# Optimization experiments

Hardware: AMD Instinct MI355X
Metric: run time of the kernel (lower is better)

The kernel has to match this reference:

```python
import jax, jax.numpy as jnp
import numpy as np
from jax import lax

C = 384        # in_channels
K = 16         # number of frames selected (self.k)
SIGMA = 0.05   # perturbation sigma (forward arg, hardcoded)
NUM_SAMPLES = 500


def setup_inputs() -> dict:
    key = jax.random.key(0)
    ks = jax.random.split(key, 8)
    B, T, N = 16, 32, 196
    D = 2 * C  # PredictorLG embed_dim for 'tpool'
    w = lambda k, s: jax.random.normal(k, s, jnp.float32) * 0.02
    return {
        "x": jax.random.normal(ks[0], (B, T * N, C), jnp.float32),
        "noise": jax.random.normal(ks[1], (B, NUM_SAMPLES, T), jnp.float32),
        "ln_g": jnp.ones((D,), jnp.float32),
        "ln_b": jnp.zeros((D,), jnp.float32),
        "w_in": w(ks[2], (D, D)), "b_in": jnp.zeros((D,), jnp.float32),
        "w1": w(ks[3], (D, D // 2)), "b1": jnp.zeros((D // 2,), jnp.float32),
        "w2": w(ks[4], (D // 2, D // 4)), "b2": jnp.zeros((D // 4,), jnp.float32),
        "w3": w(ks[5], (D // 4, 1)), "b3": jnp.zeros((1,), jnp.float32),
        "N": N, "T": T,
    }


def _predictor(x_, ln_g, ln_b, w_in, b_in, w1, b1, w2, b2, w3, b3):
    # PredictorLG: LayerNorm -> Linear -> GELU -> local/global split -> MLP -> scalar score
    mu = x_.mean(-1, keepdims=True)
    var = x_.var(-1, keepdims=True)  # biased, matches nn.LayerNorm
    h = (x_ - mu) / jnp.sqrt(var + 1e-5) * ln_g + ln_b
    h = jax.nn.gelu(h @ w_in + b_in, approximate=False)
    half = h.shape[-1] // 2
    g = h[..., half:].mean(axis=1, keepdims=True)                      # global pool over T
    h = jnp.concatenate([h[..., :half], jnp.broadcast_to(g, h[..., :half].shape)], -1)
    h = jax.nn.gelu(h @ w1 + b1, approximate=False)
    h = jax.nn.gelu(h @ w2 + b2, approximate=False)
    return (h @ w3 + b3)[..., 0]                                       # (B, T)


def reference(x, noise, ln_g, ln_b, w_in, b_in, w1, b1, w2, b2, w3, b3, N, T):
    B = x.shape[0]
    xt = x.reshape(B, T, N, C)                                         # b t n c
    x_ = jnp.concatenate([xt.mean(2), xt.max(2)], -1)                  # (B, T, 2C)
    scores = _predictor(x_, ln_g, ln_b, w_in, b_in, w1, b1, w2, b2, w3, b3)
    lo = scores.min(-1, keepdims=True)
    hi = scores.max(-1, keepdims=True)
    scores = (scores - lo) / (hi - lo + 1e-5)                          # min_max_norm
    # PerturbedTopKFunction.forward
    perturbed = scores[:, None, :] + noise * SIGMA                     # (B, ns, T)
    idx = jnp.sort(lax.top_k(perturbed, K)[1], axis=-1)                # (B, ns, K)
    indicators = jax.nn.one_hot(idx, T, dtype=x.dtype).mean(1)         # (B, K, T)
    # extract_patches_from_indicators: einsum over flattened frames
    patches = jnp.einsum('bkt,btc->bkc', indicators, xt.reshape(B, T, N * C))
    return patches.reshape(B, K * N, C)                                # 'b k (n c) -> b (k n) c'
```

## Files before the change

kernel.cpp:

```cpp
#include <hip/hip_runtime.h>
#include <math.h>

#define CC 384
#define DD 768
#define TT 32
#define NN 196
#define BB 16
#define KK 16
#define NSAMP 500
#define JV 18816
#define FRAME 75264

__device__ __forceinline__ float gelu_exact(float x) {
    return 0.5f * x * (1.0f + erff(x * 0.70710678118654752440f));
}

__global__ __launch_bounds__(384) void pool_kernel(const float* __restrict__ x,
                                                   const float* __restrict__ ln_g,
                                                   const float* __restrict__ ln_b,
                                                   float* __restrict__ xbar) {
    int row = blockIdx.x;
    const float4* xp = (const float4*)(x + (size_t)row * NN * CC);
    int tx = threadIdx.x;
    int ty = threadIdx.y;
    float4 s = make_float4(0.f, 0.f, 0.f, 0.f);
    float4 m = make_float4(-INFINITY, -INFINITY, -INFINITY, -INFINITY);
    for (int n = ty; n < NN; n += 4) {
        float4 v = xp[n * 96 + tx];
        s.x += v.x; s.y += v.y; s.z += v.z; s.w += v.w;
        m.x = fmaxf(m.x, v.x); m.y = fmaxf(m.y, v.y);
        m.z = fmaxf(m.z, v.z); m.w = fmaxf(m.w, v.w);
    }
    __shared__ float4 ssum[4][96];
    __shared__ float4 smax[4][96];
    __shared__ float xf[DD];
    ssum[ty][tx] = s;
    smax[ty][tx] = m;
    __syncthreads();
    if (ty == 0) {
        for (int r = 1; r < 4; ++r) {
            float4 a = ssum[r][tx];
            s.x += a.x; s.y += a.y; s.z += a.z; s.w += a.w;
            float4 b = smax[r][tx];
            m.x = fmaxf(m.x, b.x); m.y = fmaxf(m.y, b.y);
            m.z = fmaxf(m.z, b.z); m.w = fmaxf(m.w, b.w);
        }
        const float invn = 1.0f / (float)NN;
        xf[4*tx+0] = s.x * invn; xf[4*tx+1] = s.y * invn;
        xf[4*tx+2] = s.z * invn; xf[4*tx+3] = s.w * invn;
        xf[CC + 4*tx+0] = m.x; xf[CC + 4*tx+1] = m.y;
        xf[CC + 4*tx+2] = m.z; xf[CC + 4*tx+3] = m.w;
    }
    __syncthreads();
    int tid = ty * 96 + tx;
    float e0 = xf[tid], e1 = xf[tid + CC];
    float ps = e0 + e1, pq = e0 * e0 + e1 * e1;
    #pragma unroll
    for (int off = 32; off; off >>= 1) {
        ps += __shfl_down(ps, off);
        pq += __shfl_down(pq, off);
    }
    __shared__ float red[12];
    __shared__ float mv[2];
    int wv = tid >> 6;
    if ((tid & 63) == 0) { red[wv] = ps; red[6 + wv] = pq; }
    __syncthreads();
    if (tid == 0) {
        float su = 0.f, sq = 0.f;
        #pragma unroll
        for (int i = 0; i < 6; ++i) { su += red[i]; sq += red[6 + i]; }
        float mean = su * (1.0f / DD);
        float var  = sq * (1.0f / DD) - mean * mean;
        mv[0] = mean;
        mv[1] = rsqrtf(var + 1e-5f);
    }
    __syncthreads();
    float mean = mv[0], inv = mv[1];
    float* o = xbar + (size_t)row * DD;
    o[tid]      = (e0 - mean) * inv * ln_g[tid]      + ln_b[tid];
    o[tid + CC] = (e1 - mean) * inv * ln_g[tid + CC] + ln_b[tid + CC];
}

__global__ __launch_bounds__(1024) void fcin_kernel(const float* __restrict__ xbar,
                                                    const float* __restrict__ w_in,
                                                    const float* __restrict__ b_in,
                                                    float* __restrict__ h1,
                                                    float* __restrict__ Gpart) {
    __shared__ float xs[4][DD];
    __shared__ float pacc[4][4][256];
    int tid = threadIdx.x;
    int rowg = blockIdx.x;
    int row0 = rowg * 4;
    int col0 = blockIdx.y * 256;

    if (tid < 768) {
        int r = tid / 192, j = tid % 192;
        ((float4*)xs[r])[j] = *(const float4*)(xbar + (size_t)(row0 + r) * DD + 4 * j);
    }
    __syncthreads();

    int kg = tid >> 8;
    int c  = tid & 255;
    int col = col0 + c;
    int k0 = kg * 192;
    float a0 = 0.f, a1 = 0.f, a2 = 0.f, a3 = 0.f;
    const float* wp = w_in + (size_t)k0 * DD + col;
    #pragma unroll 2
    for (int i = 0; i < 192; i += 4) {
        float w0 = wp[(size_t)(i + 0) * DD];
        float w1v = wp[(size_t)(i + 1) * DD];
        float w2v = wp[(size_t)(i + 2) * DD];
        float w3v = wp[(size_t)(i + 3) * DD];
        float4 x0 = *(const float4*)&xs[0][k0 + i];
        float4 x1 = *(const float4*)&xs[1][k0 + i];
        float4 x2 = *(const float4*)&xs[2][k0 + i];
        float4 x3 = *(const float4*)&xs[3][k0 + i];
        a0 += x0.x * w0 + x0.y * w1v + x0.z * w2v + x0.w * w3v;
        a1 += x1.x * w0 + x1.y * w1v + x1.z * w2v + x1.w * w3v;
        a2 += x2.x * w0 + x2.y * w1v + x2.z * w2v + x2.w * w3v;
        a3 += x3.x * w0 + x3.y * w1v + x3.z * w2v + x3.w * w3v;
    }
    pacc[kg][0][c] = a0; pacc[kg][1][c] = a1;
    pacc[kg][2][c] = a2; pacc[kg][3][c] = a3;
    __syncthreads();

    int rr = tid >> 8;
    float s = b_in[col] + pacc[0][rr][c] + pacc[1][rr][c]
                        + pacc[2][rr][c] + pacc[3][rr][c];
    float g = gelu_exact(s);
    h1[(size_t)(row0 + rr) * DD + col] = g;
    pacc[0][rr][c] = g;
    __syncthreads();

    if (rr == 0 && col >= CC) {
        float gsum = pacc[0][0][c] + pacc[0][1][c] + pacc[0][2][c] + pacc[0][3][c];
        Gpart[(size_t)rowg * CC + (col - CC)] = gsum;
    }
}

__global__ __launch_bounds__(768) void mlp1_kernel(const float* __restrict__ h1,
                                                   const float* __restrict__ Gpart,
                                                   const float* __restrict__ w1,
                                                   const float* __restrict__ b1,
                                                   float* __restrict__ h2) {
    __shared__ float xs[4][CC];
    __shared__ float gs[CC];
    __shared__ float pacc[4][5][192];
    int tid = threadIdx.x;
    int rowg = blockIdx.x;
    int row0 = rowg * 4;
    int b = row0 >> 5;
    int col0 = blockIdx.y * 192;

    if (tid < CC) {
        float s = 0.f;
        const float* gp = Gpart + (size_t)(b * 8) * CC + tid;
        #pragma unroll
        for (int rg = 0; rg < 8; ++rg) s += gp[(size_t)rg * CC];
        gs[tid] = s * (1.0f / 32.0f);
    } else {
        int e = tid - CC;
        int r = e / 96, j = e % 96;
        ((float4*)xs[r])[j] = *(const float4*)(h1 + (size_t)(row0 + r) * DD + 4 * j);
    }
    __syncthreads();

    int kg = tid / 192;
    int c  = tid % 192;
    int col = col0 + c;
    int k0 = kg * 96;
    float a0 = 0.f, a1 = 0.f, a2 = 0.f, a3 = 0.f, ag = 0.f;
    const float* wl = w1 + (size_t)k0 * CC + col;
    const float* wg = w1 + (size_t)(CC + k0) * CC + col;
    #pragma unroll 2
    for (int i = 0; i < 96; i += 4) {
        float l0 = wl[(size_t)(i + 0) * CC];
        float l1 = wl[(size_t)(i + 1) * CC];
        float l2 = wl[(size_t)(i + 2) * CC];
        float l3 = wl[(size_t)(i + 3) * CC];
        float g0 = wg[(size_t)(i + 0) * CC];
        float g1 = wg[(size_t)(i + 1) * CC];
        float g2 = wg[(size_t)(i + 2) * CC];
        float g3 = wg[(size_t)(i + 3) * CC];
        float4 x0 = *(const float4*)&xs[0][k0 + i];
        float4 x1 = *(const float4*)&xs[1][k0 + i];
        float4 x2 = *(const float4*)&xs[2][k0 + i];
        float4 x3 = *(const float4*)&xs[3][k0 + i];
        float4 gv = *(const float4*)&gs[k0 + i];
        a0 += x0.x * l0 + x0.y * l1 + x0.z * l2 + x0.w * l3;
        a1 += x1.x * l0 + x1.y * l1 + x1.z * l2 + x1.w * l3;
        a2 += x2.x * l0 + x2.y * l1 + x2.z * l2 + x2.w * l3;
        a3 += x3.x * l0 + x3.y * l1 + x3.z * l2 + x3.w * l3;
        ag += gv.x * g0 + gv.y * g1 + gv.z * g2 + gv.w * g3;
    }
    pacc[kg][0][c] = a0; pacc[kg][1][c] = a1;
    pacc[kg][2][c] = a2; pacc[kg][3][c] = a3;
    pacc[kg][4][c] = ag;
    __syncthreads();

    int rr = tid / 192;
    float s = b1[col];
    #pragma unroll
    for (int kk = 0; kk < 4; ++kk)
        s += pacc[kk][rr][c] + pacc[kk][4][c];
    h2[(size_t)(row0 + rr) * CC + col] = gelu_exact(s);
}

__global__ __launch_bounds__(192) void score_kernel(const float* __restrict__ h2,
                                                    const float* __restrict__ w2,
                                                    const float* __restrict__ b2,
                                                    const float* __restrict__ w3,
                                                    float* __restrict__ scores) {
    __shared__ float h2row[CC];
    int row = blockIdx.x, tid = threadIdx.x;

    if (tid < 96)
        ((float4*)h2row)[tid] = ((const float4*)(h2 + (size_t)row * CC))[tid];
    __syncthreads();

    float a = b2[tid];
    const float* wp = w2 + tid;
    #pragma unroll 8
    for (int k = 0; k < CC; ++k)
        a += h2row[k] * wp[(size_t)k * 192];
    float v = gelu_exact(a) * w3[tid];
    #pragma unroll
    for (int off = 32; off; off >>= 1) v += __shfl_down(v, off);
    __shared__ float red[3];
    if ((tid & 63) == 0) red[tid >> 6] = v;
    __syncthreads();
    if (tid == 0) scores[row] = red[0] + red[1] + red[2];
}

__global__ __launch_bounds__(512) void topk_kernel(const float* __restrict__ scores,
                                                   const float* __restrict__ noise,
                                                   float* __restrict__ ind) {
    __shared__ float ns[TT];
    __shared__ float mnmx[2];
    __shared__ int counts[KK * TT];
    int b = blockIdx.x, tid = threadIdx.x;

    if (tid < TT) ns[tid] = scores[b * TT + tid];
    counts[tid] = 0;
    __syncthreads();
    if (tid == 0) {
        float mn = ns[0], mx = ns[0];
        for (int t = 1; t < TT; ++t) { mn = fminf(mn, ns[t]); mx = fmaxf(mx, ns[t]); }
        mnmx[0] = mn; mnmx[1] = mx;
    }
    __syncthreads();
    if (tid < TT) ns[tid] = (ns[tid] - mnmx[0]) / (mnmx[1] - mnmx[0] + 1e-5f);
    __syncthreads();

    if (tid < NSAMP) {
        const float* nb = noise + ((size_t)b * NSAMP + tid) * TT;
        float p[TT];
        #pragma unroll
        for (int t = 0; t < TT; ++t) p[t] = ns[t] + nb[t] * 0.05f;
        int k = 0;
        #pragma unroll
        for (int t = 0; t < TT; ++t) {
            int rank = 0;
            #pragma unroll
            for (int u = 0; u < TT; ++u)
                rank += (p[u] > p[t] || (p[u] == p[t] && u < t)) ? 1 : 0;
            if (rank < KK) { atomicAdd(&counts[k * TT + t], 1); ++k; }
        }
    }
    __syncthreads();
    ind[b * (KK * TT) + tid] = (float)counts[tid] * (1.0f / NSAMP);
}

__global__ __launch_bounds__(256) void gather_kernel(const float* __restrict__ x,
                                                     const float* __restrict__ ind,
                                                     float* __restrict__ out) {
    __shared__ float w[KK * TT];
    __shared__ int act[TT];
    __shared__ int nact_s;
    int b = blockIdx.y;
    int tid = threadIdx.x;
    w[tid] = ind[b * (KK * TT) + tid];
    w[256 + tid] = ind[b * (KK * TT) + 256 + tid];
    __syncthreads();
    if (tid < TT) {
        float s = 0.f;
        #pragma unroll
        for (int k = 0; k < KK; ++k) s += w[k * TT + tid];
        unsigned long long m = __ballot(s != 0.f);
        if (s != 0.f) act[__popcll(m & ((1ull << tid) - 1ull))] = tid;
        if (tid == 0) nact_s = (int)__popcll(m);
    }
    __syncthreads();
    int nact = nact_s;

    int j4 = blockIdx.x * 256 + tid;
    if (j4 >= JV) return;

    const float4* xb = (const float4*)(x + (size_t)b * TT * FRAME);
    float4 acc[KK];
    #pragma unroll
    for (int k = 0; k < KK; ++k) acc[k] = make_float4(0.f, 0.f, 0.f, 0.f);

    for (int it = 0; it < nact; ++it) {
        int t = act[it];
        float4 v = xb[(size_t)t * JV + j4];
        #pragma unroll
        for (int k = 0; k < KK; ++k) {
            float wk = w[k * TT + t];
            acc[k].x += wk * v.x; acc[k].y += wk * v.y;
            acc[k].z += wk * v.z; acc[k].w += wk * v.w;
        }
    }
    float4* ob = (float4*)(out + (size_t)b * KK * FRAME);
    #pragma unroll
    for (int k = 0; k < KK; ++k)
        ob[(size_t)k * JV + j4] = acc[k];
}

extern "C" void kernel_launch(void* const* d_in, const int* in_sizes, int n_in,
                              void* d_out, int out_size, void* d_ws, size_t ws_size,
                              hipStream_t stream) {
    const float* x     = (const float*)d_in[0];
    const float* noise = (const float*)d_in[1];
    const float* ln_g  = (const float*)d_in[2];
    const float* ln_b  = (const float*)d_in[3];
    const float* w_in  = (const float*)d_in[4];
    const float* b_in  = (const float*)d_in[5];
    const float* w1    = (const float*)d_in[6];
    const float* b1    = (const float*)d_in[7];
    const float* w2    = (const float*)d_in[8];
    const float* b2    = (const float*)d_in[9];
    const float* w3    = (const float*)d_in[10];
    const float* b3    = (const float*)d_in[11];
    (void)b3;
    float* out = (float*)d_out;

    float* ws     = (float*)d_ws;
    float* xbar   = ws;
    float* h1     = xbar + 512 * DD;
    float* Gpart  = h1 + 512 * DD;
    float* h2     = Gpart + 128 * CC;
    float* scores = h2 + 512 * CC;
    float* ind    = scores + 512;

    hipLaunchKernelGGL(pool_kernel, dim3(BB * TT), dim3(96, 4), 0, stream,
                       x, ln_g, ln_b, xbar);
    hipLaunchKernelGGL(fcin_kernel, dim3(128, 3), dim3(1024), 0, stream,
                       xbar, w_in, b_in, h1, Gpart);
    hipLaunchKernelGGL(mlp1_kernel, dim3(128, 2), dim3(768), 0, stream,
                       h1, Gpart, w1, b1, h2);
    hipLaunchKernelGGL(score_kernel, dim3(512), dim3(192), 0, stream,
                       h2, w2, b2, w3, scores);
    hipLaunchKernelGGL(topk_kernel, dim3(BB), dim3(512), 0, stream,
                       scores, noise, ind);
    hipLaunchKernelGGL(gather_kernel, dim3((JV + 255) / 256, BB), dim3(256), 0, stream,
                       x, ind, out);
}
```

Before: 120.4 us.

## Fuse MLP layers with scoring and fold top-k into gather kernel

Merges the mlp1 and score kernels into one kernel that processes two rows per block and keeps h2 in shared memory. It also moves the perturbed top-k indicator computation into every gather block, so the separate topk kernel and its ind buffer go away. The aim is to cut two kernel launches and the global round-trips for h2 and the indicators. In exchange, every gather block (74 per batch) redundantly recomputes top-k over 500 samples, and the w1 and w2 weights are re-read by each of 256 blocks.

Result: slower. 136.8 us (+13.6%).

```diff
diff --git a/kernel.cpp b/kernel.cpp
--- a/kernel.cpp
+++ b/kernel.cpp
@@ -138,19 +138,23 @@
     }
 }
 
-__global__ __launch_bounds__(768) void mlp1_kernel(const float* __restrict__ h1,
-                                                   const float* __restrict__ Gpart,
-                                                   const float* __restrict__ w1,
-                                                   const float* __restrict__ b1,
-                                                   float* __restrict__ h2) {
-    __shared__ float xs[4][CC];
+__global__ __launch_bounds__(768) void mlp1score_kernel(const float* __restrict__ h1,
+                                                        const float* __restrict__ Gpart,
+                                                        const float* __restrict__ w1,
+                                                        const float* __restrict__ b1,
+                                                        const float* __restrict__ w2,
+                                                        const float* __restrict__ b2,
+                                                        const float* __restrict__ w3,
+                                                        float* __restrict__ scores) {
     __shared__ float gs[CC];
-    __shared__ float pacc[4][5][192];
+    __shared__ float xs[2][CC];
+    __shared__ float pacc[2][3][CC];
+    __shared__ float h2s[2][CC];
+    __shared__ float sacc[2][2][192];
+    __shared__ float red[2][3];
     int tid = threadIdx.x;
-    int rowg = blockIdx.x;
-    int row0 = rowg * 4;
+    int row0 = blockIdx.x * 2;
     int b = row0 >> 5;
-    int col0 = blockIdx.y * 192;
 
     if (tid < CC) {
         float s = 0.f;
@@ -158,90 +162,95 @@
         #pragma unroll
         for (int rg = 0; rg < 8; ++rg) s += gp[(size_t)rg * CC];
         gs[tid] = s * (1.0f / 32.0f);
-    } else {
+    } else if (tid < CC + 192) {
         int e = tid - CC;
         int r = e / 96, j = e % 96;
         ((float4*)xs[r])[j] = *(const float4*)(h1 + (size_t)(row0 + r) * DD + 4 * j);
     }
     __syncthreads();
 
-    int kg = tid / 192;
-    int c  = tid % 192;
-    int col = col0 + c;
-    int k0 = kg * 96;
-    float a0 = 0.f, a1 = 0.f, a2 = 0.f, a3 = 0.f, ag = 0.f;
-    const float* wl = w1 + (size_t)k0 * CC + col;
-    const float* wg = w1 + (size_t)(CC + k0) * CC + col;
-    #pragma unroll 2
-    for (int i = 0; i < 96; i += 4) {
-        float l0 = wl[(size_t)(i + 0) * CC];
-        float l1 = wl[(size_t)(i + 1) * CC];
-        float l2 = wl[(size_t)(i + 2) * CC];
-        float l3 = wl[(size_t)(i + 3) * CC];
-        float g0 = wg[(size_t)(i + 0) * CC];
-        float g1 = wg[(size_t)(i + 1) * CC];
-        float g2 = wg[(size_t)(i + 2) * CC];
-        float g3 = wg[(size_t)(i + 3) * CC];
-        float4 x0 = *(const float4*)&xs[0][k0 + i];
-        float4 x1 = *(const float4*)&xs[1][k0 + i];
-        float4 x2 = *(const float4*)&xs[2][k0 + i];
-        float4 x3 = *(const float4*)&xs[3][k0 + i];
-        float4 gv = *(const float4*)&gs[k0 + i];
-        a0 += x0.x * l0 + x0.y * l1 + x0.z * l2 + x0.w * l3;
-        a1 += x1.x * l0 + x1.y * l1 + x1.z * l2 + x1.w * l3;
-        a2 += x2.x * l0 + x2.y * l1 + x2.z * l2 + x2.w * l3;
-        a3 += x3.x * l0 + x3.y * l1 + x3.z * l2 + x3.w * l3;
-        ag += gv.x * g0 + gv.y * g1 + gv.z * g2 + gv.w * g3;
-    }
-    pacc[kg][0][c] = a0; pacc[kg][1][c] = a1;
-    pacc[kg][2][c] = a2; pacc[kg][3][c] = a3;
-    pacc[kg][4][c] = ag;
-    __syncthreads();
-
-    int rr = tid / 192;
-    float s = b1[col];
-    #pragma unroll
-    for (int kk = 0; kk < 4; ++kk)
-        s += pacc[kk][rr][c] + pacc[kk][4][c];
-    h2[(size_t)(row0 + rr) * CC + col] = gelu_exact(s);
-}
-
-__global__ __launch_bounds__(192) void score_kernel(const float* __restrict__ h2,
-                                                    const float* __restrict__ w2,
-                                                    const float* __restrict__ b2,
-                                                    const float* __restrict__ w3,
-                                                    float* __restrict__ scores) {
-    __shared__ float h2row[CC];
-    int row = blockIdx.x, tid = threadIdx.x;
-
-    if (tid < 96)
-        ((float4*)h2row)[tid] = ((const float4*)(h2 + (size_t)row * CC))[tid];
-    __syncthreads();
-
-    float a = b2[tid];
-    const float* wp = w2 + tid;
-    #pragma unroll 8
-    for (int k = 0; k < CC; ++k)
-        a += h2row[k] * wp[(size_t)k * 192];
-    float v = gelu_exact(a) * w3[tid];
-    #pragma unroll
-    for (int off = 32; off; off >>= 1) v += __shfl_down(v, off);
-    __shared__ float red[3];
-    if ((tid & 63) == 0) red[tid >> 6] = v;
-    __syncthreads();
-    if (tid == 0) scores[row] = red[0] + red[1] + red[2];
-}
-
-__global__ __launch_bounds__(512) void topk_kernel(const float* __restrict__ scores,
-                                                   const float* __restrict__ noise,
-                                                   float* __restrict__ ind) {
+    {
+        int kg = tid / CC;
+        int col = tid % CC;
+        int k0 = kg * 192;
+        float a0 = 0.f, a1 = 0.f, ag = 0.f;
+        const float* wl = w1 + (size_t)k0 * CC + col;
+        const float* wg = w1 + (size_t)(CC + k0) * CC + col;
+        #pragma unroll 2
+        for (int i = 0; i < 192; i += 4) {
+            float l0 = wl[(size_t)(i + 0) * CC];
+            float l1 = wl[(size_t)(i + 1) * CC];
+            float l2 = wl[(size_t)(i + 2) * CC];
+            float l3 = wl[(size_t)(i + 3) * CC];
+            float g0 = wg[(size_t)(i + 0) * CC];
+            float g1 = wg[(size_t)(i + 1) * CC];
+            float g2 = wg[(size_t)(i + 2) * CC];
+            float g3 = wg[(size_t)(i + 3) * CC];
+            float4 x0 = *(const float4*)&xs[0][k0 + i];
+            float4 x1 = *(const float4*)&xs[1][k0 + i];
+            float4 gv = *(const float4*)&gs[k0 + i];
+            a0 += x0.x * l0 + x0.y * l1 + x0.z * l2 + x0.w * l3;
+            a1 += x1.x * l0 + x1.y * l1 + x1.z * l2 + x1.w * l3;
+            ag += gv.x * g0 + gv.y * g1 + gv.z * g2 + gv.w * g3;
+        }
+        pacc[kg][0][col] = a0;
+        pacc[kg][1][col] = a1;
+        pacc[kg][2][col] = ag;
+    }
+    __syncthreads();
+
+    {
+        int rr = tid / CC;
+        int c2 = tid % CC;
+        float s = b1[c2] + pacc[0][rr][c2] + pacc[1][rr][c2]
+                         + pacc[0][2][c2] + pacc[1][2][c2];
+        h2s[rr][c2] = gelu_exact(s);
+    }
+    __syncthreads();
+
+    {
+        int half = tid / 384;
+        int rr = (tid % 384) / 192;
+        int c = tid % 192;
+        int kk0 = half * 192;
+        float a = 0.f;
+        const float* wp = w2 + (size_t)kk0 * 192 + c;
+        #pragma unroll 8
+        for (int k = 0; k < 192; ++k)
+            a += h2s[rr][kk0 + k] * wp[(size_t)k * 192];
+        sacc[half][rr][c] = a;
+    }
+    __syncthreads();
+
+    if (tid < 384) {
+        int rr = tid / 192, c = tid % 192;
+        float a = sacc[0][rr][c] + sacc[1][rr][c] + b2[c];
+        float v = gelu_exact(a) * w3[c];
+        #pragma unroll
+        for (int off = 32; off; off >>= 1) v += __shfl_down(v, off);
+        if ((tid & 63) == 0) red[rr][(tid % 192) / 64] = v;
+    }
+    __syncthreads();
+    if (tid < 2)
+        scores[row0 + tid] = red[tid][0] + red[tid][1] + red[tid][2];
+}
+
+__global__ __launch_bounds__(256) void gather_kernel(const float* __restrict__ x,
+                                                     const float* __restrict__ scores,
+                                                     const float* __restrict__ noise,
+                                                     float* __restrict__ out) {
     __shared__ float ns[TT];
     __shared__ float mnmx[2];
     __shared__ int counts[KK * TT];
-    int b = blockIdx.x, tid = threadIdx.x;
-
+    __shared__ float w[KK * TT];
+    __shared__ int act[TT];
+    __shared__ int nact_s;
+    int b = blockIdx.y;
+    int tid = threadIdx.x;
+
+    counts[tid] = 0;
+    counts[tid + 256] = 0;
     if (tid < TT) ns[tid] = scores[b * TT + tid];
-    counts[tid] = 0;
     __syncthreads();
     if (tid == 0) {
         float mn = ns[0], mx = ns[0];
@@ -252,8 +261,8 @@
     if (tid < TT) ns[tid] = (ns[tid] - mnmx[0]) / (mnmx[1] - mnmx[0] + 1e-5f);
     __syncthreads();
 
-    if (tid < NSAMP) {
-        const float* nb = noise + ((size_t)b * NSAMP + tid) * TT;
+    for (int smp = tid; smp < NSAMP; smp += 256) {
+        const float* nb = noise + ((size_t)b * NSAMP + smp) * TT;
         float p[TT];
         #pragma unroll
         for (int t = 0; t < TT; ++t) p[t] = ns[t] + nb[t] * 0.05f;
@@ -268,19 +277,8 @@
         }
     }
     __syncthreads();
-    ind[b * (KK * TT) + tid] = (float)counts[tid] * (1.0f / NSAMP);
-}
-
-__global__ __launch_bounds__(256) void gather_kernel(const float* __restrict__ x,
-                                                     const float* __restrict__ ind,
-                                                     float* __restrict__ out) {
-    __shared__ float w[KK * TT];
-    __shared__ int act[TT];
-    __shared__ int nact_s;
-    int b = blockIdx.y;
-    int tid = threadIdx.x;
-    w[tid] = ind[b * (KK * TT) + tid];
-    w[256 + tid] = ind[b * (KK * TT) + 256 + tid];
+    w[tid]       = (float)counts[tid]       * (1.0f / NSAMP);
+    w[256 + tid] = (float)counts[256 + tid] * (1.0f / NSAMP);
     __syncthreads();
     if (tid < TT) {
         float s = 0.f;
@@ -339,20 +337,14 @@
     float* xbar   = ws;
     float* h1     = xbar + 512 * DD;
     float* Gpart  = h1 + 512 * DD;
-    float* h2     = Gpart + 128 * CC;
-    float* scores = h2 + 512 * CC;
-    float* ind    = scores + 512;
+    float* scores = Gpart + 128 * CC;
 
     hipLaunchKernelGGL(pool_kernel, dim3(BB * TT), dim3(96, 4), 0, stream,
                        x, ln_g, ln_b, xbar);
     hipLaunchKernelGGL(fcin_kernel, dim3(128, 3), dim3(1024), 0, stream,
                        xbar, w_in, b_in, h1, Gpart);
-    hipLaunchKernelGGL(mlp1_kernel, dim3(128, 2), dim3(768), 0, stream,
-                       h1, Gpart, w1, b1, h2);
-    hipLaunchKernelGGL(score_kernel, dim3(512), dim3(192), 0, stream,
-                       h2, w2, b2, w3, scores);
-    hipLaunchKernelGGL(topk_kernel, dim3(BB), dim3(512), 0, stream,
-                       scores, noise, ind);
+    hipLaunchKernelGGL(mlp1score_kernel, dim3(256), dim3(768), 0, stream,
+                       h1, Gpart, w1, b1, w2, b2, w3, scores);
     hipLaunchKernelGGL(gather_kernel, dim3((JV + 255) / 256, BB), dim3(256), 0, stream,
-                       x, ind, out);
-}
+                       x, scores, noise, out);
+}
```
